# Kernel optimization log

Hardware: AMD Instinct MI355X
Metric: run time of the kernel (lower is better)

## Reference

```python
import jax, jax.numpy as jnp
import numpy as np
import math

H = 1024      # hidden_size
S = 512       # num_sent (attention length)
TOPK = 5
BATCH = 160   # base_batch(32) * TOPK
STEPS = 4     # prior decode steps
NEG = -1e10


def setup_inputs() -> dict:
    key = jax.random.key(0)
    ks = jax.random.split(key, 20)
    sc = 1.0 / math.sqrt(H)
    return {
        'last_hidden': jax.random.normal(ks[0], (1, BATCH, H), jnp.float32),
        'decoder_inputs': jax.random.normal(ks[1], (BATCH, 1, H), jnp.float32),
        'encoder_outputs': jax.random.normal(ks[2], (BATCH, S, H), jnp.float32),
        'attention_scores': jax.random.normal(ks[3], (STEPS, BATCH, 1, S), jnp.float32),
        'attention_mask': jnp.zeros((BATCH, 1, S), jnp.float32),
        'evidence_scores': jax.random.uniform(ks[4], (BATCH,), jnp.float32),
        'evidence_sentence_index': jax.random.randint(ks[5], (BATCH, STEPS), 0, S),
        'W1': jax.random.normal(ks[6], (H, H), jnp.float32) * sc,
        'b1': jnp.zeros((H,), jnp.float32),
        'W2': jax.random.normal(ks[7], (H, H), jnp.float32) * sc,
        'b2': jnp.zeros((H,), jnp.float32),
        'W3': jax.random.normal(ks[8], (H, 2 * H), jnp.float32) * sc,
        'b3': jnp.zeros((H,), jnp.float32),
        'W_ih': jax.random.normal(ks[9], (3 * H, H), jnp.float32) * sc,
        'W_hh': jax.random.normal(ks[10], (3 * H, H), jnp.float32) * sc,
        'b_ih': jnp.zeros((3 * H,), jnp.float32),
        'b_hh': jnp.zeros((3 * H,), jnp.float32),
    }


def _gru_step(x, h, W_ih, W_hh, b_ih, b_hh):
    # x, h: (batch, H); torch GRU gate order: r, z, n
    gi = x @ W_ih.T + b_ih
    gh = h @ W_hh.T + b_hh
    gi_r, gi_z, gi_n = jnp.split(gi, 3, axis=-1)
    gh_r, gh_z, gh_n = jnp.split(gh, 3, axis=-1)
    r = jax.nn.sigmoid(gi_r + gh_r)
    z = jax.nn.sigmoid(gi_z + gh_z)
    n = jnp.tanh(gi_n + r * gh_n)
    return (1.0 - z) * n + z * h


def reference(last_hidden, decoder_inputs, encoder_outputs, attention_scores,
              attention_mask, evidence_scores, evidence_sentence_index,
              W1, b1, W2, b2, W3, b3, W_ih, W_hh, b_ih, b_hh):
    batch = decoder_inputs.shape[0]
    topk = TOPK
    base = batch // topk

    key_enc = encoder_outputs @ W1.T + b1          # (b, S, H)
    val_enc = encoder_outputs @ W2.T + b2          # (b, S, H)

    h_new = _gru_step(decoder_inputs[:, 0, :], last_hidden[0], W_ih, W_hh, b_ih, b_hh)
    output = h_new[:, None, :]                      # (b, 1, H)

    attn_outputs = (jnp.einsum('bh,bsh->bs', h_new, key_enc) / math.sqrt(H))[:, None, :] + attention_mask  # (b,1,S)
    attn_alignment = jax.nn.softmax(attn_outputs, axis=-1)
    context = jnp.einsum('bos,bsh->boh', attn_alignment, val_enc)  # (b,1,H)
    result = jnp.concatenate([context, output], axis=-1) @ W3.T + b3  # (b,1,H)

    # top-k candidates per beam
    scores, sentences = jax.lax.top_k(attn_alignment[:, 0, :], topk)  # (b, topk)
    log_scores = -jnp.log(scores) + evidence_scores[:, None]          # (b, topk)

    # beam rerank: pick topk smallest among topk*topk per base batch (stable ascending sort)
    ls = log_scores.reshape(base, topk * topk)
    order = jnp.argsort(ls, axis=-1)[:, :topk]      # (base, topk)
    s_local = order // topk
    r_sel = order % topk
    s_flat = (s_local + jnp.arange(base)[:, None] * topk).reshape(-1)  # (b,) source beam idx
    r_flat = r_sel.reshape(-1)

    new_evidence_scores = log_scores[s_flat, r_flat]          # (b,)
    new_sentences = sentences[s_flat, r_flat]                 # (b,)
    result_new = result[s_flat]                               # (b,1,H)
    hidden_new = h_new[s_flat][None]                          # (1,b,H)
    attn_out_new = attn_outputs[s_flat]                       # (b,1,S)
    attn_scores_new = jnp.concatenate([attention_scores[:, s_flat], attn_out_new[None]], axis=0)  # (steps+1,b,1,S)
    ev_idx_new = jnp.concatenate(
        [evidence_sentence_index[s_flat], new_sentences[:, None].astype(evidence_sentence_index.dtype)], axis=1)
    mask_new = attention_mask[s_flat].at[jnp.arange(batch), 0, new_sentences].set(NEG)

    return (result_new, hidden_new, ev_idx_new, attn_scores_new, mask_new, new_evidence_scores)
```

## Files before the change

kernel.cpp:

```cpp
#include <hip/hip_runtime.h>
#include <cstddef>

#define NEGC (-10000000000.0f)


template <bool NT, int AMODE>
__device__ __forceinline__ void gemm_body2(const float* __restrict__ A, int pcount,
                                           const float* __restrict__ bias,
                                           const float* __restrict__ scale,
                                           const float* __restrict__ W, int ldw, int woff,
                                           float* __restrict__ Co, int N, int Ktot,
                                           int n0, int z, int zcount) {
  __shared__ float As[160][36];
  __shared__ float Ws[64][36];
  const int KL = Ktot / zcount;
  const int kbase = z * KL;
  const int tid = threadIdx.x;
  const int tx = tid & 15, ty = tid >> 4;
  float acc[10][4];
#pragma unroll
  for (int i = 0; i < 10; ++i)
#pragma unroll
    for (int j = 0; j < 4; ++j) acc[i][j] = 0.f;

  for (int kt = 0; kt < KL; kt += 32) {
    const int kg = kbase + kt;
    for (int i = tid; i < 160 * 32; i += 256) {
      int m = i >> 5, kk = i & 31;
      float v;
      if (AMODE == 0) {
        v = A[(size_t)m * 1024 + kg + kk];
      } else if (AMODE == 1) {
        v = bias[kg + kk];
        for (int p = 0; p < pcount; ++p)
          v += A[(size_t)p * 163840 + (size_t)m * 1024 + kg + kk];
      } else {
        v = 0.f;
        for (int p = 0; p < pcount; ++p)
          v += A[(size_t)p * 163840 + (size_t)m * 1024 + kg + kk];
        v *= scale[m];
      }
      As[m][kk] = v;
    }
    if (NT) {
      for (int i = tid; i < 64 * 32; i += 256) {
        int n = i >> 5, kk = i & 31;
        Ws[n][kk] = W[(size_t)(n0 + n) * ldw + woff + kg + kk];
      }
    } else {
      for (int i = tid; i < 64 * 32; i += 256) {
        int kk = i >> 6, n = i & 63;
        Ws[n][kk] = W[(size_t)(kg + kk) * ldw + n0 + n];
      }
    }
    __syncthreads();
    for (int kk = 0; kk < 32; kk += 4) {
      float4 a[10], w[4];
#pragma unroll
      for (int i = 0; i < 10; ++i)
        a[i] = *reinterpret_cast<const float4*>(&As[ty + 16 * i][kk]);
#pragma unroll
      for (int j = 0; j < 4; ++j)
        w[j] = *reinterpret_cast<const float4*>(&Ws[tx + 16 * j][kk]);
#pragma unroll
      for (int i = 0; i < 10; ++i)
#pragma unroll
        for (int j = 0; j < 4; ++j) {
          acc[i][j] += a[i].x * w[j].x;
          acc[i][j] += a[i].y * w[j].y;
          acc[i][j] += a[i].z * w[j].z;
          acc[i][j] += a[i].w * w[j].w;
        }
    }
    __syncthreads();
  }
  float* Cb = Co + (size_t)z * 160 * N + n0;
#pragma unroll
  for (int i = 0; i < 10; ++i)
#pragma unroll
    for (int j = 0; j < 4; ++j)
      Cb[(size_t)(ty + 16 * i) * N + tx + 16 * j] = acc[i][j];
}

__global__ __launch_bounds__(256) void k_gemm_gru(const float* __restrict__ X,
                                                  const float* __restrict__ H0,
                                                  const float* __restrict__ Wih,
                                                  const float* __restrict__ Whh,
                                                  float* __restrict__ GIp,
                                                  float* __restrict__ GHp) {
  const float* A = blockIdx.z ? H0 : X;
  const float* W = blockIdx.z ? Whh : Wih;
  float* C = blockIdx.z ? GHp : GIp;
  gemm_body2<true, 0>(A, 0, nullptr, nullptr, W, 1024, 0, C, 3072, 1024,
                      blockIdx.x * 64, blockIdx.y, gridDim.y);
}

__global__ __launch_bounds__(256) void k_gemm_qw3b(const float* __restrict__ h,
                                                   const float* __restrict__ W1,
                                                   const float* __restrict__ W3,
                                                   float* __restrict__ qp,
                                                   float* __restrict__ respB) {
  if (blockIdx.z == 0)
    gemm_body2<false, 0>(h, 0, nullptr, nullptr, W1, 1024, 0, qp, 1024, 1024,
                         blockIdx.x * 64, blockIdx.y, gridDim.y);
  else
    gemm_body2<true, 0>(h, 0, nullptr, nullptr, W3, 2048, 1024, respB, 1024, 1024,
                        blockIdx.x * 64, blockIdx.y, gridDim.y);
}

__global__ __launch_bounds__(256) void k_gemm_w2(const float* __restrict__ ctxep,
                                                 const float* __restrict__ invZ,
                                                 const float* __restrict__ W2,
                                                 float* __restrict__ ctxp) {
  gemm_body2<true, 2>(ctxep, 4, nullptr, invZ, W2, 1024, 0, ctxp, 1024, 1024,
                      blockIdx.x * 64, blockIdx.y, gridDim.y);
}

__global__ __launch_bounds__(256) void k_gemm_w3a(const float* __restrict__ ctxp,
                                                  const float* __restrict__ b2,
                                                  const float* __restrict__ W3,
                                                  float* __restrict__ resp) {
  gemm_body2<true, 1>(ctxp, 8, b2, nullptr, W3, 2048, 0, resp, 1024, 1024,
                      blockIdx.x * 64, blockIdx.y, gridDim.y);
}

__global__ __launch_bounds__(256) void gru_k(const float* __restrict__ GIp,
                                             const float* __restrict__ GHp,
                                             const float* __restrict__ bih,
                                             const float* __restrict__ bhh,
                                             const float* __restrict__ hprev,
                                             const float* __restrict__ b1,
                                             float* __restrict__ h_new,
                                             float* __restrict__ hb1) {
  int b = blockIdx.x, t = threadIdx.x;
  float dot = 0.f;
#pragma unroll
  for (int u = 0; u < 4; ++u) {
    int h = t + 256 * u;
    float gir = bih[h], giz = bih[1024 + h], gin = bih[2048 + h];
    float ghr = bhh[h], ghz = bhh[1024 + h], ghn = bhh[2048 + h];
#pragma unroll
    for (int z = 0; z < 8; ++z) {
      size_t base = ((size_t)z * 160 + b) * 3072 + h;
      gir += GIp[base]; giz += GIp[base + 1024]; gin += GIp[base + 2048];
      ghr += GHp[base]; ghz += GHp[base + 1024]; ghn += GHp[base + 2048];
    }
    float r = 1.0f / (1.0f + expf(-(gir + ghr)));
    float zg = 1.0f / (1.0f + expf(-(giz + ghz)));
    float n = tanhf(gin + r * ghn);
    float hp = hprev[(size_t)b * 1024 + h];
    float hn = (1.0f - zg) * n + zg * hp;
    h_new[(size_t)b * 1024 + h] = hn;
    dot += hn * b1[h];
  }
  __shared__ float red[256];
  red[t] = dot; __syncthreads();
  for (int o = 128; o > 0; o >>= 1) { if (t < o) red[t] += red[t + o]; __syncthreads(); }
  if (t == 0) hb1[b] = red[0];
}

__global__ __launch_bounds__(256) void fused_enc_k(const float* __restrict__ enc,
                                                   const float* __restrict__ qp,
                                                   const float* __restrict__ hb1,
                                                   const float* __restrict__ maskin,
                                                   float* __restrict__ attn,
                                                   float* __restrict__ ctxep) {
  int b = blockIdx.x, c = blockIdx.y;
  int tid = threadIdx.x, wave = tid >> 6, lane = tid & 63;
  __shared__ float4 et[8 * 256];
  __shared__ float4 qs[256];
  float4 qa = {0.f, 0.f, 0.f, 0.f};
#pragma unroll
  for (int z = 0; z < 8; ++z) {
    const float4 tq = *reinterpret_cast<const float4*>(&qp[((size_t)z * 160 + b) * 1024 + 4 * tid]);
    qa.x += tq.x; qa.y += tq.y; qa.z += tq.z; qa.w += tq.w;
  }
  qs[tid] = qa;
  __syncthreads();
  float4 q[4];
#pragma unroll
  for (int j = 0; j < 4; ++j) q[j] = qs[lane + 64 * j];
  float hb = hb1[b] * 0.03125f;
  float4 acc[4];
#pragma unroll
  for (int j = 0; j < 4; ++j) acc[j] = make_float4(0.f, 0.f, 0.f, 0.f);

  const float4* encb = reinterpret_cast<const float4*>(enc) + ((size_t)b * 512 + c * 128) * 256;
  for (int it = 0; it < 16; ++it) {
    __syncthreads();
    const float4* src = encb + (size_t)it * 8 * 256;
#pragma unroll
    for (int u = 0; u < 8; ++u) et[u * 256 + tid] = src[u * 256 + tid];
    __syncthreads();
#pragma unroll
    for (int u = 0; u < 2; ++u) {
      int r = 2 * wave + u;
      float4 e[4];
#pragma unroll
      for (int j = 0; j < 4; ++j) e[j] = et[r * 256 + lane + 64 * j];
      float d = 0.f;
#pragma unroll
      for (int j = 0; j < 4; ++j)
        d += e[j].x * q[j].x + e[j].y * q[j].y + e[j].z * q[j].z + e[j].w * q[j].w;
#pragma unroll
      for (int off = 32; off > 0; off >>= 1) d += __shfl_xor(d, off);
      int s = c * 128 + it * 8 + r;
      float sc = d * 0.03125f + hb + maskin[(size_t)b * 512 + s];
      if (lane == 0) attn[(size_t)b * 512 + s] = sc;
      float w = expf(sc);
#pragma unroll
      for (int j = 0; j < 4; ++j) {
        acc[j].x += w * e[j].x; acc[j].y += w * e[j].y;
        acc[j].z += w * e[j].z; acc[j].w += w * e[j].w;
      }
    }
  }
  __syncthreads();
  float4* red = et;
#pragma unroll
  for (int j = 0; j < 4; ++j) {
    red[wave * 64 + lane] = acc[j];
    __syncthreads();
    if (wave == 0) {
      float4 r0 = red[lane], r1 = red[64 + lane], r2 = red[128 + lane], r3 = red[192 + lane];
      float4 rr;
      rr.x = r0.x + r1.x + r2.x + r3.x;
      rr.y = r0.y + r1.y + r2.y + r3.y;
      rr.z = r0.z + r1.z + r2.z + r3.z;
      rr.w = r0.w + r1.w + r2.w + r3.w;
      reinterpret_cast<float4*>(ctxep)[((size_t)c * 160 + b) * 256 + lane + 64 * j] = rr;
    }
    __syncthreads();
  }
}

__global__ __launch_bounds__(256) void smtopk_k(const float* __restrict__ attn,
                                                const float* __restrict__ ev,
                                                float* __restrict__ invZ,
                                                float* __restrict__ logsc,
                                                int* __restrict__ sent) {
  int b = blockIdx.x, t = threadIdx.x;
  __shared__ float v[512];
  __shared__ float red[256];
  __shared__ int redi[256];
  float x0 = attn[(size_t)b * 512 + t], x1 = attn[(size_t)b * 512 + 256 + t];
  v[t] = x0; v[t + 256] = x1;
  red[t] = fmaxf(x0, x1); __syncthreads();
  for (int o = 128; o > 0; o >>= 1) { if (t < o) red[t] = fmaxf(red[t], red[t + o]); __syncthreads(); }
  float mx = red[0]; __syncthreads();
  red[t] = expf(x0 - mx) + expf(x1 - mx); __syncthreads();
  for (int o = 128; o > 0; o >>= 1) { if (t < o) red[t] += red[t + o]; __syncthreads(); }
  float Z = red[0]; __syncthreads();
  red[t] = expf(x0) + expf(x1); __syncthreads();
  for (int o = 128; o > 0; o >>= 1) { if (t < o) red[t] += red[t + o]; __syncthreads(); }
  if (t == 0) invZ[b] = 1.0f / red[0];
  __syncthreads();
  for (int r = 0; r < 5; ++r) {
    float bv; int bi;
    float v0 = v[t], v1 = v[t + 256];
    if (v1 > v0) { bv = v1; bi = t + 256; } else { bv = v0; bi = t; }
    red[t] = bv; redi[t] = bi; __syncthreads();
    for (int o = 128; o > 0; o >>= 1) {
      if (t < o) {
        if (red[t + o] > red[t] || (red[t + o] == red[t] && redi[t + o] < redi[t])) {
          red[t] = red[t + o]; redi[t] = redi[t + o];
        }
      }
      __syncthreads();
    }
    if (t == 0) {
      int id = redi[0];
      float a = expf(red[0] - mx) / Z;
      sent[b * 5 + r] = id;
      logsc[b * 5 + r] = -logf(a) + ev[b];
      v[id] = -3e38f;
    }
    __syncthreads();
  }
}

__global__ void beam_k(const float* __restrict__ logsc, const int* __restrict__ sent,
                       const int* __restrict__ evidx_in, int* __restrict__ s_flat,
                       int* __restrict__ new_sent, float* __restrict__ out) {
  int g = blockIdx.x;
  int lane = threadIdx.x;
  float val = 1e30f;
  if (lane < 25) val = logsc[(g * 5 + lane / 5) * 5 + (lane % 5)];
  for (int j = 0; j < 5; ++j) {
    float bv = val; int bi = lane;
#pragma unroll
    for (int off = 1; off < 64; off <<= 1) {
      float ov = __shfl_xor(bv, off);
      int oi = __shfl_xor(bi, off);
      if (ov < bv || (ov == bv && oi < bi)) { bv = ov; bi = oi; }
    }
    if (lane == 0) {
      int ii = bi / 5, rr = bi % 5;
      int bp = g * 5 + j, sf = g * 5 + ii;
      s_flat[bp] = sf;
      int ns = sent[sf * 5 + rr];
      new_sent[bp] = ns;
      out[820000 + bp] = bv;
      for (int tt = 0; tt < 4; ++tt)
        out[327680 + bp * 5 + tt] = (float)evidx_in[sf * 4 + tt];
      out[327680 + bp * 5 + 4] = (float)ns;
    }
    if (lane == bi) val = 1e30f;
  }
}

__global__ void pack_k(const float* __restrict__ resp, const float* __restrict__ b3,
                       const float* __restrict__ h_new, const float* __restrict__ attn_sc_in,
                       const float* __restrict__ attn, const float* __restrict__ mask_in,
                       const int* __restrict__ s_flat, const int* __restrict__ new_sent,
                       float* __restrict__ out) {
  int idx = blockIdx.x * 256 + threadIdx.x;
  if (idx < 163840) {
    int bp = idx >> 10, k = idx & 1023;
    int sf = s_flat[bp];
    float v = b3[k];
#pragma unroll
    for (int z = 0; z < 16; ++z) v += resp[(size_t)z * 163840 + (size_t)sf * 1024 + k];
    out[idx] = v;
  } else if (idx < 327680) {
    int rel = idx - 163840;
    int bp = rel >> 10, k = rel & 1023;
    out[idx] = h_new[(size_t)s_flat[bp] * 1024 + k];
  } else if (idx < 737280) {
    int rel = idx - 327680;
    int t = rel / 81920, r2 = rel % 81920;
    int bp = r2 >> 9, s = r2 & 511;
    int sf = s_flat[bp];
    float v = (t < 4) ? attn_sc_in[((size_t)t * 160 + sf) * 512 + s]
                      : attn[(size_t)sf * 512 + s];
    out[328480 + rel] = v;
  } else {
    int rel = idx - 737280;
    int bp = rel >> 9, s = rel & 511;
    int sf = s_flat[bp];
    float v = (s == new_sent[bp]) ? NEGC : mask_in[(size_t)sf * 512 + s];
    out[738080 + rel] = v;
  }
}

extern "C" void kernel_launch(void* const* d_in, const int* in_sizes, int n_in,
                              void* d_out, int out_size, void* d_ws, size_t ws_size,
                              hipStream_t stream) {
  const float* last_hidden = (const float*)d_in[0];
  const float* dec_in      = (const float*)d_in[1];
  const float* enc         = (const float*)d_in[2];
  const float* attn_sc_in  = (const float*)d_in[3];
  const float* mask_in     = (const float*)d_in[4];
  const float* ev          = (const float*)d_in[5];
  const int*   evidx       = (const int*)d_in[6];
  const float* W1  = (const float*)d_in[7];
  const float* b1  = (const float*)d_in[8];
  const float* W2  = (const float*)d_in[9];
  const float* b2  = (const float*)d_in[10];
  const float* W3  = (const float*)d_in[11];
  const float* b3  = (const float*)d_in[12];
  const float* Wih = (const float*)d_in[13];
  const float* Whh = (const float*)d_in[14];
  const float* bih = (const float*)d_in[15];
  const float* bhh = (const float*)d_in[16];
  float* out = (float*)d_out;
  float* ws = (float*)d_ws;

  float* GIp   = ws;
  float* GHp   = ws + 3932160;
  float* resp  = ws;
  float* respB = resp + 8 * 163840;
  float* ctxp  = GHp;
  float* qp    = ws + 7864320;
  float* ctxep = ws + 9175040;
  float* h_new = ws + 9830400;
  float* hb1   = ws + 9994240;
  float* attn  = ws + 9994400;
  float* invZ  = ws + 10076320;
  float* logsc = ws + 10076480;
  int* sent     = (int*)(ws + 10077280);
  int* s_flat   = sent + 800;
  int* new_sent = s_flat + 160;

  k_gemm_gru<<<dim3(48, 8, 2), dim3(256), 0, stream>>>(dec_in, last_hidden, Wih, Whh, GIp, GHp);
  gru_k<<<dim3(160), dim3(256), 0, stream>>>(GIp, GHp, bih, bhh, last_hidden, b1, h_new, hb1);
  k_gemm_qw3b<<<dim3(16, 8, 2), dim3(256), 0, stream>>>(h_new, W1, W3, qp, respB);
  fused_enc_k<<<dim3(160, 4), dim3(256), 0, stream>>>(enc, qp, hb1, mask_in, attn, ctxep);
  smtopk_k<<<dim3(160), dim3(256), 0, stream>>>(attn, ev, invZ, logsc, sent);
  beam_k<<<dim3(32), dim3(64), 0, stream>>>(logsc, sent, evidx, s_flat, new_sent, out);
  k_gemm_w2<<<dim3(16, 8), dim3(256), 0, stream>>>(ctxep, invZ, W2, ctxp);
  k_gemm_w3a<<<dim3(16, 8), dim3(256), 0, stream>>>(ctxp, b2, W3, resp);
  pack_k<<<dim3(3200), dim3(256), 0, stream>>>(resp, b3, h_new, attn_sc_in, attn, mask_in,
                                               s_flat, new_sent, out);
}
```

Baseline: 322.9 us.

## Vectorize GEMM tile loads, stream encoder rows via registers, fuse softmax-topk with beam

```diff
diff --git a/kernel.cpp b/kernel.cpp
--- a/kernel.cpp
+++ b/kernel.cpp
@@ -5,14 +5,14 @@
 
 
 template <bool NT, int AMODE>
-__device__ __forceinline__ void gemm_body2(const float* __restrict__ A, int pcount,
+__device__ __forceinline__ void gemm_body3(const float* __restrict__ A, int pcount,
                                            const float* __restrict__ bias,
                                            const float* __restrict__ scale,
                                            const float* __restrict__ W, int ldw, int woff,
                                            float* __restrict__ Co, int N, int Ktot,
                                            int n0, int z, int zcount) {
-  __shared__ float As[160][36];
-  __shared__ float Ws[64][36];
+  __shared__ float As[160][44];
+  __shared__ float Ws[64][44];
   const int KL = Ktot / zcount;
   const int kbase = z * KL;
   const int tid = threadIdx.x;
@@ -25,27 +25,33 @@
 
   for (int kt = 0; kt < KL; kt += 32) {
     const int kg = kbase + kt;
-    for (int i = tid; i < 160 * 32; i += 256) {
-      int m = i >> 5, kk = i & 31;
-      float v;
+#pragma unroll
+    for (int k5 = 0; k5 < 5; ++k5) {
+      int i = tid + 256 * k5;
+      int m = i >> 3, c4 = i & 7;
+      float4 v;
       if (AMODE == 0) {
-        v = A[(size_t)m * 1024 + kg + kk];
-      } else if (AMODE == 1) {
-        v = bias[kg + kk];
-        for (int p = 0; p < pcount; ++p)
-          v += A[(size_t)p * 163840 + (size_t)m * 1024 + kg + kk];
+        v = *reinterpret_cast<const float4*>(&A[(size_t)m * 1024 + kg + 4 * c4]);
       } else {
-        v = 0.f;
-        for (int p = 0; p < pcount; ++p)
-          v += A[(size_t)p * 163840 + (size_t)m * 1024 + kg + kk];
-        v *= scale[m];
-      }
-      As[m][kk] = v;
+        if (AMODE == 1) v = *reinterpret_cast<const float4*>(&bias[kg + 4 * c4]);
+        else v = make_float4(0.f, 0.f, 0.f, 0.f);
+        for (int p = 0; p < pcount; ++p) {
+          float4 t = *reinterpret_cast<const float4*>(
+              &A[(size_t)p * 163840 + (size_t)m * 1024 + kg + 4 * c4]);
+          v.x += t.x; v.y += t.y; v.z += t.z; v.w += t.w;
+        }
+        if (AMODE == 2) { float s = scale[m]; v.x *= s; v.y *= s; v.z *= s; v.w *= s; }
+      }
+      *reinterpret_cast<float4*>(&As[m][4 * c4]) = v;
     }
     if (NT) {
-      for (int i = tid; i < 64 * 32; i += 256) {
-        int n = i >> 5, kk = i & 31;
-        Ws[n][kk] = W[(size_t)(n0 + n) * ldw + woff + kg + kk];
+#pragma unroll
+      for (int k2 = 0; k2 < 2; ++k2) {
+        int i = tid + 256 * k2;
+        int n = i >> 3, c4 = i & 7;
+        float4 v = *reinterpret_cast<const float4*>(
+            &W[(size_t)(n0 + n) * ldw + woff + kg + 4 * c4]);
+        *reinterpret_cast<float4*>(&Ws[n][4 * c4]) = v;
       }
     } else {
       for (int i = tid; i < 64 * 32; i += 256) {
@@ -91,7 +97,7 @@
   const float* A = blockIdx.z ? H0 : X;
   const float* W = blockIdx.z ? Whh : Wih;
   float* C = blockIdx.z ? GHp : GIp;
-  gemm_body2<true, 0>(A, 0, nullptr, nullptr, W, 1024, 0, C, 3072, 1024,
+  gemm_body3<true, 0>(A, 0, nullptr, nullptr, W, 1024, 0, C, 3072, 1024,
                       blockIdx.x * 64, blockIdx.y, gridDim.y);
 }
 
@@ -101,10 +107,10 @@
                                                    float* __restrict__ qp,
                                                    float* __restrict__ respB) {
   if (blockIdx.z == 0)
-    gemm_body2<false, 0>(h, 0, nullptr, nullptr, W1, 1024, 0, qp, 1024, 1024,
+    gemm_body3<false, 0>(h, 0, nullptr, nullptr, W1, 1024, 0, qp, 1024, 1024,
                          blockIdx.x * 64, blockIdx.y, gridDim.y);
   else
-    gemm_body2<true, 0>(h, 0, nullptr, nullptr, W3, 2048, 1024, respB, 1024, 1024,
+    gemm_body3<true, 0>(h, 0, nullptr, nullptr, W3, 2048, 1024, respB, 1024, 1024,
                         blockIdx.x * 64, blockIdx.y, gridDim.y);
 }
 
@@ -112,7 +118,7 @@
                                                  const float* __restrict__ invZ,
                                                  const float* __restrict__ W2,
                                                  float* __restrict__ ctxp) {
-  gemm_body2<true, 2>(ctxep, 4, nullptr, invZ, W2, 1024, 0, ctxp, 1024, 1024,
+  gemm_body3<true, 2>(ctxep, 8, nullptr, invZ, W2, 1024, 0, ctxp, 1024, 1024,
                       blockIdx.x * 64, blockIdx.y, gridDim.y);
 }
 
@@ -120,7 +126,7 @@
                                                   const float* __restrict__ b2,
                                                   const float* __restrict__ W3,
                                                   float* __restrict__ resp) {
-  gemm_body2<true, 1>(ctxp, 8, b2, nullptr, W3, 2048, 0, resp, 1024, 1024,
+  gemm_body3<true, 1>(ctxp, 8, b2, nullptr, W3, 2048, 0, resp, 1024, 1024,
                       blockIdx.x * 64, blockIdx.y, gridDim.y);
 }
 
@@ -159,21 +165,20 @@
   if (t == 0) hb1[b] = red[0];
 }
 
-__global__ __launch_bounds__(256) void fused_enc_k(const float* __restrict__ enc,
-                                                   const float* __restrict__ qp,
-                                                   const float* __restrict__ hb1,
-                                                   const float* __restrict__ maskin,
-                                                   float* __restrict__ attn,
-                                                   float* __restrict__ ctxep) {
+__global__ __launch_bounds__(256) void enc_k(const float* __restrict__ enc,
+                                             const float* __restrict__ qp,
+                                             const float* __restrict__ hb1,
+                                             const float* __restrict__ maskin,
+                                             float* __restrict__ attn,
+                                             float* __restrict__ ctxep) {
   int b = blockIdx.x, c = blockIdx.y;
   int tid = threadIdx.x, wave = tid >> 6, lane = tid & 63;
-  __shared__ float4 et[8 * 256];
   __shared__ float4 qs[256];
   float4 qa = {0.f, 0.f, 0.f, 0.f};
 #pragma unroll
   for (int z = 0; z < 8; ++z) {
-    const float4 tq = *reinterpret_cast<const float4*>(&qp[((size_t)z * 160 + b) * 1024 + 4 * tid]);
-    qa.x += tq.x; qa.y += tq.y; qa.z += tq.z; qa.w += tq.w;
+    float4 t = *reinterpret_cast<const float4*>(&qp[((size_t)z * 160 + b) * 1024 + 4 * tid]);
+    qa.x += t.x; qa.y += t.y; qa.z += t.z; qa.w += t.w;
   }
   qs[tid] = qa;
   __syncthreads();
@@ -185,38 +190,39 @@
 #pragma unroll
   for (int j = 0; j < 4; ++j) acc[j] = make_float4(0.f, 0.f, 0.f, 0.f);
 
-  const float4* encb = reinterpret_cast<const float4*>(enc) + ((size_t)b * 512 + c * 128) * 256;
-  for (int it = 0; it < 16; ++it) {
-    __syncthreads();
-    const float4* src = encb + (size_t)it * 8 * 256;
-#pragma unroll
-    for (int u = 0; u < 8; ++u) et[u * 256 + tid] = src[u * 256 + tid];
-    __syncthreads();
-#pragma unroll
-    for (int u = 0; u < 2; ++u) {
-      int r = 2 * wave + u;
-      float4 e[4];
-#pragma unroll
-      for (int j = 0; j < 4; ++j) e[j] = et[r * 256 + lane + 64 * j];
+  int row0 = c * 64 + wave * 16;
+  const float4* encb = reinterpret_cast<const float4*>(enc) + ((size_t)b * 512 + row0) * 256;
+  const float* mrow = &maskin[(size_t)b * 512 + row0];
+  float* arow = &attn[(size_t)b * 512 + row0];
+
+  for (int it = 0; it < 4; ++it) {
+    float4 e[4][4];
+#pragma unroll
+    for (int r = 0; r < 4; ++r)
+#pragma unroll
+      for (int j = 0; j < 4; ++j)
+        e[r][j] = encb[(size_t)(it * 4 + r) * 256 + lane + 64 * j];
+#pragma unroll
+    for (int r = 0; r < 4; ++r) {
       float d = 0.f;
 #pragma unroll
       for (int j = 0; j < 4; ++j)
-        d += e[j].x * q[j].x + e[j].y * q[j].y + e[j].z * q[j].z + e[j].w * q[j].w;
+        d += e[r][j].x * q[j].x + e[r][j].y * q[j].y + e[r][j].z * q[j].z + e[r][j].w * q[j].w;
 #pragma unroll
       for (int off = 32; off > 0; off >>= 1) d += __shfl_xor(d, off);
-      int s = c * 128 + it * 8 + r;
-      float sc = d * 0.03125f + hb + maskin[(size_t)b * 512 + s];
-      if (lane == 0) attn[(size_t)b * 512 + s] = sc;
+      int s = it * 4 + r;
+      float sc = d * 0.03125f + hb + mrow[s];
+      if (lane == 0) arow[s] = sc;
       float w = expf(sc);
 #pragma unroll
       for (int j = 0; j < 4; ++j) {
-        acc[j].x += w * e[j].x; acc[j].y += w * e[j].y;
-        acc[j].z += w * e[j].z; acc[j].w += w * e[j].w;
+        acc[j].x += w * e[r][j].x; acc[j].y += w * e[r][j].y;
+        acc[j].z += w * e[r][j].z; acc[j].w += w * e[r][j].w;
       }
     }
   }
   __syncthreads();
-  float4* red = et;
+  float4* red = qs;
 #pragma unroll
   for (int j = 0; j < 4; ++j) {
     red[wave * 64 + lane] = acc[j];
@@ -234,78 +240,82 @@
   }
 }
 
-__global__ __launch_bounds__(256) void smtopk_k(const float* __restrict__ attn,
-                                                const float* __restrict__ ev,
-                                                float* __restrict__ invZ,
-                                                float* __restrict__ logsc,
-                                                int* __restrict__ sent) {
-  int b = blockIdx.x, t = threadIdx.x;
+__global__ __launch_bounds__(256) void smtopk_beam_k(const float* __restrict__ attn,
+                                                     const float* __restrict__ ev,
+                                                     const int* __restrict__ evidx_in,
+                                                     float* __restrict__ invZ,
+                                                     int* __restrict__ s_flat,
+                                                     int* __restrict__ new_sent,
+                                                     float* __restrict__ out) {
+  int g = blockIdx.x, t = threadIdx.x;
   __shared__ float v[512];
   __shared__ float red[256];
   __shared__ int redi[256];
-  float x0 = attn[(size_t)b * 512 + t], x1 = attn[(size_t)b * 512 + 256 + t];
-  v[t] = x0; v[t + 256] = x1;
-  red[t] = fmaxf(x0, x1); __syncthreads();
-  for (int o = 128; o > 0; o >>= 1) { if (t < o) red[t] = fmaxf(red[t], red[t + o]); __syncthreads(); }
-  float mx = red[0]; __syncthreads();
-  red[t] = expf(x0 - mx) + expf(x1 - mx); __syncthreads();
-  for (int o = 128; o > 0; o >>= 1) { if (t < o) red[t] += red[t + o]; __syncthreads(); }
-  float Z = red[0]; __syncthreads();
-  red[t] = expf(x0) + expf(x1); __syncthreads();
-  for (int o = 128; o > 0; o >>= 1) { if (t < o) red[t] += red[t + o]; __syncthreads(); }
-  if (t == 0) invZ[b] = 1.0f / red[0];
+  __shared__ float lsc[25];
+  __shared__ int snt[25];
+
+  for (int i = 0; i < 5; ++i) {
+    int b = g * 5 + i;
+    float x0 = attn[(size_t)b * 512 + t], x1 = attn[(size_t)b * 512 + 256 + t];
+    v[t] = x0; v[t + 256] = x1;
+    red[t] = fmaxf(x0, x1); __syncthreads();
+    for (int o = 128; o > 0; o >>= 1) { if (t < o) red[t] = fmaxf(red[t], red[t + o]); __syncthreads(); }
+    float mx = red[0]; __syncthreads();
+    red[t] = expf(x0 - mx) + expf(x1 - mx); __syncthreads();
+    for (int o = 128; o > 0; o >>= 1) { if (t < o) red[t] += red[t + o]; __syncthreads(); }
+    float Z = red[0]; __syncthreads();
+    red[t] = expf(x0) + expf(x1); __syncthreads();
+    for (int o = 128; o > 0; o >>= 1) { if (t < o) red[t] += red[t + o]; __syncthreads(); }
+    if (t == 0) invZ[b] = 1.0f / red[0];
+    __syncthreads();
+    float evb = ev[b];
+    for (int r = 0; r < 5; ++r) {
+      float bv; int bi;
+      float v0 = v[t], v1 = v[t + 256];
+      if (v1 > v0) { bv = v1; bi = t + 256; } else { bv = v0; bi = t; }
+      red[t] = bv; redi[t] = bi; __syncthreads();
+      for (int o = 128; o > 0; o >>= 1) {
+        if (t < o) {
+          if (red[t + o] > red[t] || (red[t + o] == red[t] && redi[t + o] < redi[t])) {
+            red[t] = red[t + o]; redi[t] = redi[t + o];
+          }
+        }
+        __syncthreads();
+      }
+      if (t == 0) {
+        int id = redi[0];
+        float a = expf(red[0] - mx) / Z;
+        snt[i * 5 + r] = id;
+        lsc[i * 5 + r] = -logf(a) + evb;
+        v[id] = -3e38f;
+      }
+      __syncthreads();
+    }
+  }
   __syncthreads();
-  for (int r = 0; r < 5; ++r) {
-    float bv; int bi;
-    float v0 = v[t], v1 = v[t + 256];
-    if (v1 > v0) { bv = v1; bi = t + 256; } else { bv = v0; bi = t; }
-    red[t] = bv; redi[t] = bi; __syncthreads();
-    for (int o = 128; o > 0; o >>= 1) {
-      if (t < o) {
-        if (red[t + o] > red[t] || (red[t + o] == red[t] && redi[t + o] < redi[t])) {
-          red[t] = red[t + o]; redi[t] = redi[t + o];
-        }
-      }
-      __syncthreads();
-    }
-    if (t == 0) {
-      int id = redi[0];
-      float a = expf(red[0] - mx) / Z;
-      sent[b * 5 + r] = id;
-      logsc[b * 5 + r] = -logf(a) + ev[b];
-      v[id] = -3e38f;
-    }
-    __syncthreads();
-  }
-}
-
-__global__ void beam_k(const float* __restrict__ logsc, const int* __restrict__ sent,
-                       const int* __restrict__ evidx_in, int* __restrict__ s_flat,
-                       int* __restrict__ new_sent, float* __restrict__ out) {
-  int g = blockIdx.x;
-  int lane = threadIdx.x;
-  float val = 1e30f;
-  if (lane < 25) val = logsc[(g * 5 + lane / 5) * 5 + (lane % 5)];
-  for (int j = 0; j < 5; ++j) {
-    float bv = val; int bi = lane;
-#pragma unroll
-    for (int off = 1; off < 64; off <<= 1) {
-      float ov = __shfl_xor(bv, off);
-      int oi = __shfl_xor(bi, off);
-      if (ov < bv || (ov == bv && oi < bi)) { bv = ov; bi = oi; }
-    }
-    if (lane == 0) {
-      int ii = bi / 5, rr = bi % 5;
-      int bp = g * 5 + j, sf = g * 5 + ii;
-      s_flat[bp] = sf;
-      int ns = sent[sf * 5 + rr];
-      new_sent[bp] = ns;
-      out[820000 + bp] = bv;
-      for (int tt = 0; tt < 4; ++tt)
-        out[327680 + bp * 5 + tt] = (float)evidx_in[sf * 4 + tt];
-      out[327680 + bp * 5 + 4] = (float)ns;
-    }
-    if (lane == bi) val = 1e30f;
+  if (t < 64) {
+    float val = (t < 25) ? lsc[(t / 5) * 5 + (t % 5)] : 1e30f;
+    for (int j = 0; j < 5; ++j) {
+      float bv = val; int bi = t;
+#pragma unroll
+      for (int off = 1; off < 64; off <<= 1) {
+        float ov = __shfl_xor(bv, off);
+        int oi = __shfl_xor(bi, off);
+        if (ov < bv || (ov == bv && oi < bi)) { bv = ov; bi = oi; }
+      }
+      if (t == 0) {
+        int ii = bi / 5, rr = bi % 5;
+        int bp = g * 5 + j, sf = g * 5 + ii;
+        s_flat[bp] = sf;
+        int ns = snt[ii * 5 + rr];
+        new_sent[bp] = ns;
+        out[820000 + bp] = bv;
+        for (int tt = 0; tt < 4; ++tt)
+          out[327680 + bp * 5 + tt] = (float)evidx_in[sf * 4 + tt];
+        out[327680 + bp * 5 + 4] = (float)ns;
+      }
+      if (t == bi) val = 1e30f;
+    }
   }
 }
 
@@ -373,21 +383,18 @@
   float* ctxp  = GHp;
   float* qp    = ws + 7864320;
   float* ctxep = ws + 9175040;
-  float* h_new = ws + 9830400;
-  float* hb1   = ws + 9994240;
-  float* attn  = ws + 9994400;
-  float* invZ  = ws + 10076320;
-  float* logsc = ws + 10076480;
-  int* sent     = (int*)(ws + 10077280);
-  int* s_flat   = sent + 800;
+  float* h_new = ws + 10485760;
+  float* hb1   = ws + 10649600;
+  float* attn  = ws + 10649760;
+  float* invZ  = ws + 10731680;
+  int* s_flat   = (int*)(ws + 10731840);
   int* new_sent = s_flat + 160;
 
   k_gemm_gru<<<dim3(48, 8, 2), dim3(256), 0, stream>>>(dec_in, last_hidden, Wih, Whh, GIp, GHp);
   gru_k<<<dim3(160), dim3(256), 0, stream>>>(GIp, GHp, bih, bhh, last_hidden, b1, h_new, hb1);
   k_gemm_qw3b<<<dim3(16, 8, 2), dim3(256), 0, stream>>>(h_new, W1, W3, qp, respB);
-  fused_enc_k<<<dim3(160, 4), dim3(256), 0, stream>>>(enc, qp, hb1, mask_in, attn, ctxep);
-  smtopk_k<<<dim3(160), dim3(256), 0, stream>>>(attn, ev, invZ, logsc, sent);
-  beam_k<<<dim3(32), dim3(64), 0, stream>>>(logsc, sent, evidx, s_flat, new_sent, out);
+  enc_k<<<dim3(160, 8), dim3(256), 0, stream>>>(enc, qp, hb1, mask_in, attn, ctxep);
+  smtopk_beam_k<<<dim3(32), dim3(256), 0, stream>>>(attn, ev, evidx, invZ, s_flat, new_sent, out);
   k_gemm_w2<<<dim3(16, 8), dim3(256), 0, stream>>>(ctxep, invZ, W2, ctxp);
   k_gemm_w3a<<<dim3(16, 8), dim3(256), 0, stream>>>(ctxp, b2, W3, resp);
   pack_k<<<dim3(3200), dim3(256), 0, stream>>>(resp, b3, h_new, attn_sc_in, attn, mask_in,
```

New measurement: 279.0 us. 13.6% less time.
